# Optimization experiments

Measured on AMD Instinct MI355X. Metric: run time of the kernel, lower is better.

## Reference

```python
import jax, jax.numpy as jnp
import numpy as np

N_NODES = 10000
N_EDGES = 320000
K = 5
C_IN = 128
C_OUT = 128


def setup_inputs() -> dict:
    key = jax.random.key(0)
    k_h, k_x, k_w, k_b = jax.random.split(key, 4)
    h = jax.random.normal(k_h, (N_NODES, C_IN), dtype=jnp.float32)
    X = jax.random.normal(k_x, (N_EDGES, K), dtype=jnp.float32)
    weight = jax.random.normal(k_w, (K, C_IN, C_OUT), dtype=jnp.float32) * 0.05
    bias = jax.random.normal(k_b, (C_OUT,), dtype=jnp.float32)
    # Unique (src, dst) pairs so scatter-set == segment-sum (matches torch indexing assignment).
    rng = np.random.default_rng(0)
    lin = np.unique(rng.integers(0, N_NODES * N_NODES, size=int(N_EDGES * 1.3)))
    assert len(lin) >= N_EDGES
    lin = lin[:N_EDGES]
    edge_index = jnp.asarray(np.stack([lin // N_NODES, lin % N_NODES]), dtype=jnp.int64)
    batch_node = jnp.zeros((N_NODES,), dtype=jnp.float32)
    return {"h": h, "X": X, "edge_index": edge_index, "batch_node": batch_node,
            "weight": weight, "bias": bias}


def reference(h, X, edge_index, batch_node, weight, bias):
    # Original torch code scatters X.T into a dense (K, N, N) adjacency and does
    # res = A @ h; that equals, per order k:
    #   res[k, i, :] = sum_{e: src_e = i} X[e, k] * h[dst_e, :]
    # which we compute sparsely with segment_sum (edges are unique).
    N = h.shape[0]
    src = edge_index[0]
    dst = edge_index[1]
    h_dst = h[dst]  # [E, C_in] gathered destination features

    def per_k(xk):  # xk: [E] edge values for one order k
        return jax.ops.segment_sum(xk[:, None] * h_dst, src, num_segments=N)  # [N, C_in]

    res_k = jax.vmap(per_k, in_axes=1)(X)  # [K, N, C_in]
    out = jnp.einsum('kni,kio->no', res_k, weight) + bias  # [N, C_out]
    return out
```

## Files before the change

### kernel.cpp

```cpp
#include <hip/hip_runtime.h>

#define N_NODES 10000
#define N_EDGES 320000
#define KDIM 640
#define C_OUT 128

typedef __attribute__((ext_vector_type(8))) short short8;
typedef __attribute__((ext_vector_type(4))) float floatx4;
typedef __attribute__((ext_vector_type(2))) unsigned int uintx2;

__device__ __forceinline__ unsigned short f2bf(float f) {
    unsigned int b = __float_as_uint(f);
    b = (b + 0x7FFFu + ((b >> 16) & 1u)) >> 16;
    return (unsigned short)b;
}
__device__ __forceinline__ unsigned int pack2(float x, float y) {
    return (unsigned int)f2bf(x) | ((unsigned int)f2bf(y) << 16);
}
__device__ __forceinline__ float2 unpack2(unsigned int u) {
    float2 r;
    r.x = __uint_as_float(u << 16);
    r.y = __uint_as_float(u & 0xFFFF0000u);
    return r;
}

__global__ __launch_bounds__(256) void prep(
        const float* __restrict__ h, uintx2* __restrict__ hb4,
        const float* __restrict__ W, unsigned short* __restrict__ Wt,
        const int* __restrict__ src, int* __restrict__ offsets) {
    const int bid = blockIdx.x;
    const int tid = threadIdx.x;

    if (bid < 1250) {
        const int t = bid * 256 + tid;
        floatx4 v = __builtin_nontemporal_load(&((const floatx4*)h)[t]);
        uintx2 o;
        o.x = pack2(v.x, v.y);
        o.y = pack2(v.z, v.w);
        hb4[t] = o;
    } else if (bid < 1330) {
        __shared__ float tile[32][33];
        const int b = bid - 1250;
        const int k0 = (b % 20) * 32, o0 = (b / 20) * 32;
        const int tx = tid & 31, ty = tid >> 5;
#pragma unroll
        for (int i = 0; i < 4; ++i)
            tile[ty + 8 * i][tx] =
                __builtin_nontemporal_load(&W[(size_t)(k0 + ty + 8 * i) * C_OUT + o0 + tx]);
        __syncthreads();
#pragma unroll
        for (int i = 0; i < 4; ++i)
            Wt[(size_t)(o0 + ty + 8 * i) * KDIM + k0 + tx] = f2bf(tile[tx][ty + 8 * i]);
    } else {
        const int n = (bid - 1330) * 256 + tid;
        if (n > N_NODES) return;
        int lo = 0, hi = N_EDGES;
        while (lo < hi) {
            int mid = (lo + hi) >> 1;
            if (src[mid] < n) lo = mid + 1; else hi = mid;
        }
        offsets[n] = lo;
    }
}

__global__ __launch_bounds__(512, 4) void fused_spectconv(
        const unsigned int* __restrict__ h2,
        const float* __restrict__ X,
        const int* __restrict__ dst,
        const int* __restrict__ offsets,
        const unsigned short* __restrict__ Wt,
        const float* __restrict__ bias,
        float* __restrict__ out) {
    __shared__ unsigned short Rs[16][648];

    const int tid  = threadIdx.x;
    const int wv   = __builtin_amdgcn_readfirstlane(tid >> 6);
    const int lane = tid & 63;
    const int m0   = blockIdx.x * 16;

    for (int nn = 0; nn < 2; ++nn) {
        const int node = m0 + wv * 2 + nn;
        const int e0 = offsets[node];
        const int e1 = offsets[node + 1];

        float a0x=0,a0y=0, a1x=0,a1y=0, a2x=0,a2y=0, a3x=0,a3y=0, a4x=0,a4y=0;

        int e = e0;
        for (; e + 3 < e1; e += 4) {
            const int d0 = dst[e + 0];
            const int d1 = dst[e + 1];
            const int d2 = dst[e + 2];
            const int d3 = dst[e + 3];
            const unsigned int u0 = h2[(size_t)d0 * 64 + lane];
            const unsigned int u1 = h2[(size_t)d1 * 64 + lane];
            const unsigned int u2 = h2[(size_t)d2 * 64 + lane];
            const unsigned int u3 = h2[(size_t)d3 * 64 + lane];
#pragma unroll
            for (int q = 0; q < 4; ++q) {
                const unsigned int u = (q == 0) ? u0 : (q == 1) ? u1 : (q == 2) ? u2 : u3;
                const float* Xp = X + (size_t)(e + q) * 5;
                const float x0 = Xp[0], x1 = Xp[1], x2 = Xp[2], x3 = Xp[3], x4 = Xp[4];
                const float2 hv = unpack2(u);
                a0x = fmaf(x0, hv.x, a0x); a0y = fmaf(x0, hv.y, a0y);
                a1x = fmaf(x1, hv.x, a1x); a1y = fmaf(x1, hv.y, a1y);
                a2x = fmaf(x2, hv.x, a2x); a2y = fmaf(x2, hv.y, a2y);
                a3x = fmaf(x3, hv.x, a3x); a3y = fmaf(x3, hv.y, a3y);
                a4x = fmaf(x4, hv.x, a4x); a4y = fmaf(x4, hv.y, a4y);
            }
        }
        for (; e < e1; ++e) {
            const int d = dst[e];
            const unsigned int u = h2[(size_t)d * 64 + lane];
            const float* Xp = X + (size_t)e * 5;
            const float x0 = Xp[0], x1 = Xp[1], x2 = Xp[2], x3 = Xp[3], x4 = Xp[4];
            const float2 hv = unpack2(u);
            a0x = fmaf(x0, hv.x, a0x); a0y = fmaf(x0, hv.y, a0y);
            a1x = fmaf(x1, hv.x, a1x); a1y = fmaf(x1, hv.y, a1y);
            a2x = fmaf(x2, hv.x, a2x); a2y = fmaf(x2, hv.y, a2y);
            a3x = fmaf(x3, hv.x, a3x); a3y = fmaf(x3, hv.y, a3y);
            a4x = fmaf(x4, hv.x, a4x); a4y = fmaf(x4, hv.y, a4y);
        }

        const int nrel = wv * 2 + nn;
        *(unsigned int*)&Rs[nrel][0 * 128 + 2 * lane] = pack2(a0x, a0y);
        *(unsigned int*)&Rs[nrel][1 * 128 + 2 * lane] = pack2(a1x, a1y);
        *(unsigned int*)&Rs[nrel][2 * 128 + 2 * lane] = pack2(a2x, a2y);
        *(unsigned int*)&Rs[nrel][3 * 128 + 2 * lane] = pack2(a3x, a3y);
        *(unsigned int*)&Rs[nrel][4 * 128 + 2 * lane] = pack2(a4x, a4y);
    }

    __syncthreads();

    const int col  = lane & 15;
    const int quad = lane >> 4;
    const int c0   = wv * 16;

    floatx4 acc = {0.f, 0.f, 0.f, 0.f};
    const unsigned short* wrow = Wt + (size_t)(c0 + col) * KDIM + quad * 8;

#pragma unroll
    for (int kc = 0; kc < 20; ++kc) {
        const short8 af = *(const short8*)&Rs[col][kc * 32 + quad * 8];
        const short8 bf = *(const short8*)(wrow + kc * 32);
        acc = __builtin_amdgcn_mfma_f32_16x16x32_bf16(af, bf, acc, 0, 0, 0);
    }

    const float bv = bias[c0 + col];
#pragma unroll
    for (int r = 0; r < 4; ++r) {
        const int m = m0 + quad * 4 + r;
        __builtin_nontemporal_store(acc[r] + bv, &out[(size_t)m * C_OUT + c0 + col]);
    }
}

extern "C" void kernel_launch(void* const* d_in, const int* in_sizes, int n_in,
                              void* d_out, int out_size, void* d_ws, size_t ws_size,
                              hipStream_t stream) {
    const float* h      = (const float*)d_in[0];
    const float* X      = (const float*)d_in[1];
    const int*   ei     = (const int*)d_in[2];
    const float* weight = (const float*)d_in[4];
    const float* bias   = (const float*)d_in[5];
    float* out = (float*)d_out;

    const int* src = ei;
    const int* dst = ei + N_EDGES;

    char* wsb = (char*)d_ws;
    int*            offsets = (int*)wsb;
    uintx2*         hb4     = (uintx2*)(wsb + (64 << 10));
    unsigned short* Wtb     = (unsigned short*)(wsb + (64 << 10) + (4 << 20));

    prep<<<1370, 256, 0, stream>>>(h, hb4, weight, Wtb, src, offsets);
    fused_spectconv<<<625, 512, 0, stream>>>((const unsigned int*)hb4, X, dst,
                                             offsets, Wtb, bias, out);
}
```

Baseline: 106.0 us.

## Unroll edge gather to 8 and stage weight chunks through shared memory

The edge aggregation loop now gathers 8 destination rows per iteration instead of 4, putting more independent loads in flight to hide gather latency. The MFMA stage now cooperatively copies the bf16 weight matrix in 64-wide K chunks into a padded shared-memory tile, instead of each wave reading its weight rows directly from global memory. The weight staging adds 10 chunk iterations with about 20 block barriers and extra LDS use, which may lower occupancy. Register pressure also rises from the wider unroll.

```diff
diff --git a/kernel.cpp b/kernel.cpp
--- a/kernel.cpp
+++ b/kernel.cpp
@@ -72,6 +72,7 @@
         const float* __restrict__ bias,
         float* __restrict__ out) {
     __shared__ unsigned short Rs[16][648];
+    __shared__ unsigned short Bs[128][68];
 
     const int tid  = threadIdx.x;
     const int wv   = __builtin_amdgcn_readfirstlane(tid >> 6);
@@ -86,21 +87,19 @@
         float a0x=0,a0y=0, a1x=0,a1y=0, a2x=0,a2y=0, a3x=0,a3y=0, a4x=0,a4y=0;
 
         int e = e0;
-        for (; e + 3 < e1; e += 4) {
-            const int d0 = dst[e + 0];
-            const int d1 = dst[e + 1];
-            const int d2 = dst[e + 2];
-            const int d3 = dst[e + 3];
-            const unsigned int u0 = h2[(size_t)d0 * 64 + lane];
-            const unsigned int u1 = h2[(size_t)d1 * 64 + lane];
-            const unsigned int u2 = h2[(size_t)d2 * 64 + lane];
-            const unsigned int u3 = h2[(size_t)d3 * 64 + lane];
+        for (; e + 7 < e1; e += 8) {
+            int d[8];
+            unsigned int u[8];
 #pragma unroll
-            for (int q = 0; q < 4; ++q) {
-                const unsigned int u = (q == 0) ? u0 : (q == 1) ? u1 : (q == 2) ? u2 : u3;
+            for (int q = 0; q < 8; ++q) d[q] = dst[e + q];
+#pragma unroll
+            for (int q = 0; q < 8; ++q)
+                u[q] = h2[(size_t)d[q] * 64 + lane];
+#pragma unroll
+            for (int q = 0; q < 8; ++q) {
                 const float* Xp = X + (size_t)(e + q) * 5;
                 const float x0 = Xp[0], x1 = Xp[1], x2 = Xp[2], x3 = Xp[3], x4 = Xp[4];
-                const float2 hv = unpack2(u);
+                const float2 hv = unpack2(u[q]);
                 a0x = fmaf(x0, hv.x, a0x); a0y = fmaf(x0, hv.y, a0y);
                 a1x = fmaf(x1, hv.x, a1x); a1y = fmaf(x1, hv.y, a1y);
                 a2x = fmaf(x2, hv.x, a2x); a2y = fmaf(x2, hv.y, a2y);
@@ -136,13 +135,25 @@
     const int c0   = wv * 16;
 
     floatx4 acc = {0.f, 0.f, 0.f, 0.f};
-    const unsigned short* wrow = Wt + (size_t)(c0 + col) * KDIM + quad * 8;
 
 #pragma unroll
-    for (int kc = 0; kc < 20; ++kc) {
-        const short8 af = *(const short8*)&Rs[col][kc * 32 + quad * 8];
-        const short8 bf = *(const short8*)(wrow + kc * 32);
-        acc = __builtin_amdgcn_mfma_f32_16x16x32_bf16(af, bf, acc, 0, 0, 0);
+    for (int chunk = 0; chunk < 10; ++chunk) {
+        if (chunk) __syncthreads();
+#pragma unroll
+        for (int r = 0; r < 2; ++r) {
+            const int c = r * 512 + tid;
+            const int row = c >> 3, c8 = c & 7;
+            *(short8*)&Bs[row][c8 * 8] =
+                *(const short8*)(Wt + (size_t)row * KDIM + chunk * 64 + c8 * 8);
+        }
+        __syncthreads();
+
+#pragma unroll
+        for (int hh = 0; hh < 2; ++hh) {
+            const short8 af = *(const short8*)&Rs[col][chunk * 64 + hh * 32 + quad * 8];
+            const short8 bf = *(const short8*)&Bs[c0 + col][hh * 32 + quad * 8];
+            acc = __builtin_amdgcn_mfma_f32_16x16x32_bf16(af, bf, acc, 0, 0, 0);
+        }
     }
 
     const float bv = bias[c0 + col];
```

Result: faster. 100.2 us (-5.5%).
